# Kernel tuning notes

Measured on AMD Instinct MI355X. Metric: run time of the kernel, lower is better.

Reference implementation:

```python
import math
import jax, jax.numpy as jnp
import numpy as np

DIM = 1024
DIM_HEAD = 64
NUM_HEAD = 16
HIDDEN = DIM_HEAD * NUM_HEAD  # 1024
B, L = 4, 2048
EPS = 1e-12  # torch F.normalize eps


def rms_norm(x, g):
    # F.normalize(x, dim=-1) * g * sqrt(d): L2-normalize then rescale
    d = x.shape[-1]
    norm = jnp.maximum(jnp.linalg.norm(x, axis=-1, keepdims=True), EPS)
    return x / norm * g * math.sqrt(d)


def setup_inputs() -> dict:
    key = jax.random.key(0)
    ks = jax.random.split(key, 8)
    x = jax.random.normal(ks[0], (B, L, DIM), dtype=jnp.float32)
    # torch Linear init scale ~ 1/sqrt(fan_in)
    s1 = 1.0 / math.sqrt(DIM)
    s2 = 1.0 / math.sqrt(HIDDEN)
    Wqkv = jax.random.uniform(ks[1], (3 * HIDDEN, DIM), minval=-s1, maxval=s1, dtype=jnp.float32)
    bqkv = jax.random.uniform(ks[2], (3 * HIDDEN,), minval=-s1, maxval=s1, dtype=jnp.float32)
    Wout = jax.random.uniform(ks[3], (DIM, HIDDEN), minval=-s2, maxval=s2, dtype=jnp.float32)
    bout = jax.random.uniform(ks[4], (DIM,), minval=-s2, maxval=s2, dtype=jnp.float32)
    g_q = jnp.ones((HIDDEN,), dtype=jnp.float32)
    g_k = jnp.ones((HIDDEN,), dtype=jnp.float32)
    g_out = jnp.ones((DIM,), dtype=jnp.float32)
    return {"x": x, "Wqkv": Wqkv, "bqkv": bqkv, "Wout": Wout, "bout": bout,
            "g_q": g_q, "g_k": g_k, "g_out": g_out}


def reference(x, Wqkv, bqkv, Wout, bout, g_q, g_k, g_out):
    scale = DIM_HEAD ** -0.5
    qkv = x @ Wqkv.T + bqkv  # (b, l, 3*hidden)
    q, k, v = jnp.split(qkv, 3, axis=-1)
    # QK RMSNorm applied over flattened (num_head*d) channel dim
    q = rms_norm(q, g_q)
    k = rms_norm(k, g_k)
    split_heads = lambda t: t.reshape(B, L, NUM_HEAD, DIM_HEAD).transpose(0, 2, 1, 3)
    q, k, v = split_heads(q), split_heads(k), split_heads(v)  # (b, h, l, d)
    q = q * scale
    sim = jnp.einsum('bhld,bhnd->bhln', q, k)
    attn = jax.nn.softmax(sim, axis=-1)
    out = jnp.einsum('bhln,bhnd->bhld', attn, v)  # (b, h, l, d)
    out = out.transpose(0, 2, 1, 3).reshape(B, L, HIDDEN)  # b l (h d)
    out = out @ Wout.T + bout
    return rms_norm(out, g_out)
```

## Files before the change

### kernel.cpp

```cpp
#include <hip/hip_runtime.h>
#include <math.h>

#define DIM       1024
#define DIM_HEAD  64
#define NUM_HEAD  16
#define HIDDEN    1024
#define BATCH     4
#define SEQ       2048
#define ROWS      (BATCH * SEQ)
#define QKV_N     (3 * HIDDEN)
#define QK_N      2048

typedef __bf16 bf16_t;
typedef __bf16 bf16x8 __attribute__((ext_vector_type(8)));
typedef __bf16 bf16x4 __attribute__((ext_vector_type(4)));
typedef float  f32x4  __attribute__((ext_vector_type(4)));

#define F32_ONE_PATTERN 0x3F800000u
#define LOG2E 1.44269504088896f

#define GLOAD_LDS16(gp, lp)                                                  \
    __builtin_amdgcn_global_load_lds(                                        \
        (const __attribute__((address_space(1))) void*)(const void*)(gp),    \
        (__attribute__((address_space(3))) void*)(void*)(lp), 16, 0, 0)

__global__ __launch_bounds__(256) void decode_bf16(const void* __restrict__ in,
                                                   bf16_t* __restrict__ out,
                                                   const unsigned* __restrict__ sniff,
                                                   long n)
{
    const bool isf32 = (*sniff == F32_ONE_PATTERN);
    const long i = ((long)blockIdx.x * 256 + threadIdx.x) * 8;
    if (i >= n) return;
    if (isf32) {
        const float* p = (const float*)in + i;
        f32x4 a = *(const f32x4*)p;
        f32x4 b = *(const f32x4*)(p + 4);
        bf16x8 r;
        r[0] = (bf16_t)a[0]; r[1] = (bf16_t)a[1]; r[2] = (bf16_t)a[2]; r[3] = (bf16_t)a[3];
        r[4] = (bf16_t)b[0]; r[5] = (bf16_t)b[1]; r[6] = (bf16_t)b[2]; r[7] = (bf16_t)b[3];
        *(bf16x8*)&out[i] = r;
    } else {
        *(bf16x8*)&out[i] = *(const bf16x8*)((const bf16_t*)in + i);
    }
}

__global__ __launch_bounds__(256) void decode_params(
    const void* __restrict__ bqkv_raw, const void* __restrict__ bout_raw,
    const void* __restrict__ gq_raw,   const void* __restrict__ gk_raw,
    const void* __restrict__ gout_raw,
    float* __restrict__ o_bqkv, float* __restrict__ o_bout,
    float* __restrict__ o_gq,   float* __restrict__ o_gk,
    float* __restrict__ o_gout,
    const unsigned* __restrict__ sniff)
{
    const bool isf32 = (*sniff == F32_ONE_PATTERN);
    const int blk = blockIdx.x;
    const void* src; float* dst; int off;
    if (blk < 3)       { src = bqkv_raw; dst = o_bqkv; off = blk * 1024; }
    else if (blk == 3) { src = bout_raw; dst = o_bout; off = 0; }
    else if (blk == 4) { src = gq_raw;   dst = o_gq;   off = 0; }
    else if (blk == 5) { src = gk_raw;   dst = o_gk;   off = 0; }
    else               { src = gout_raw; dst = o_gout; off = 0; }
    const int i = off + threadIdx.x * 4;
    if (isf32) {
        *(f32x4*)&dst[i] = *((const f32x4*)src + (off >> 2) + threadIdx.x);
    } else {
        bf16x4 v = *((const bf16x4*)src + (off >> 2) + threadIdx.x);
        f32x4 a;
        a[0] = (float)v[0]; a[1] = (float)v[1]; a[2] = (float)v[2]; a[3] = (float)v[3];
        *(f32x4*)&dst[i] = a;
    }
}

__global__ __launch_bounds__(256) void gemm_qkv(
    const bf16_t* __restrict__ A,
    const bf16_t* __restrict__ Bt,
    const float*  __restrict__ bias,
    bf16_t* __restrict__ qk,
    bf16_t* __restrict__ vt)
{
    __shared__ __align__(16) bf16_t smem[8704];
    bf16_t* const As = smem;
    bf16_t* const Bs = smem + 4096;
    bf16_t* const Ts = smem;

    const int tid  = threadIdx.x;
    const int w    = tid >> 6;
    const int lane = tid & 63;
    const int wr   = w >> 1;
    const int wc   = w & 1;
    const int lr   = lane & 15;
    const int quad = lane >> 4;

    const int m0 = blockIdx.y * 128;
    const int n0 = blockIdx.x * 128;
    const int K  = DIM;

    const int e0 = tid * 8;
    const int r0 = e0 >> 5;
    const int c0 = e0 & 31;
    const int r1 = r0 + 64;

    f32x4 acc[4][4];
    #pragma unroll
    for (int i = 0; i < 4; i++)
        #pragma unroll
        for (int j = 0; j < 4; j++)
            acc[i][j] = (f32x4){0.f, 0.f, 0.f, 0.f};

    const bf16_t* pa0 = &A [(size_t)(m0 + r0) * K + c0];
    const bf16_t* pa1 = &A [(size_t)(m0 + r1) * K + c0];
    const bf16_t* pb0 = &Bt[(size_t)(n0 + r0) * K + c0];
    const bf16_t* pb1 = &Bt[(size_t)(n0 + r1) * K + c0];

    for (int k0 = 0; k0 < K; k0 += 32) {
        __syncthreads();
        GLOAD_LDS16(pa0 + k0, &As[e0]);
        GLOAD_LDS16(pa1 + k0, &As[e0 + 2048]);
        GLOAD_LDS16(pb0 + k0, &Bs[e0]);
        GLOAD_LDS16(pb1 + k0, &Bs[e0 + 2048]);
        __syncthreads();

        bf16x8 af[4], bfr[4];
        #pragma unroll
        for (int i = 0; i < 4; i++)
            af[i] = *(const bf16x8*)&As[(wr * 64 + i * 16 + lr) * 32 + quad * 8];
        #pragma unroll
        for (int j = 0; j < 4; j++)
            bfr[j] = *(const bf16x8*)&Bs[(wc * 64 + j * 16 + lr) * 32 + quad * 8];
        #pragma unroll
        for (int i = 0; i < 4; i++)
            #pragma unroll
            for (int j = 0; j < 4; j++)
                acc[i][j] = __builtin_amdgcn_mfma_f32_16x16x32_bf16(
                    af[i], bfr[j], acc[i][j], 0, 0, 0);
    }

    if (n0 < 2048) {
        #pragma unroll
        for (int i = 0; i < 4; i++) {
            const int row = m0 + wr * 64 + i * 16 + quad * 4;
            #pragma unroll
            for (int j = 0; j < 4; j++) {
                const int col = n0 + wc * 64 + j * 16 + lr;
                const float bv = bias[col];
                f32x4 v = acc[i][j];
                #pragma unroll
                for (int r = 0; r < 4; r++)
                    qk[(size_t)(row + r) * QK_N + col] = (bf16_t)(v[r] + bv);
            }
        }
    } else {
        const int b      = m0 >> 11;
        const int l_base = m0 & 2047;
        const int c_base = n0 - 2048;
        #pragma unroll
        for (int p = 0; p < 2; p++) {
            __syncthreads();
            if (wc == p) {
                #pragma unroll
                for (int j = 0; j < 4; j++) {
                    const int c = j * 16 + lr;
                    const float bv = bias[2048 + c_base + p * 64 + c];
                    #pragma unroll
                    for (int i = 0; i < 4; i++) {
                        const int l = wr * 64 + i * 16 + quad * 4;
                        f32x4 v = acc[i][j];
                        bf16x4 o;
                        o[0] = (bf16_t)(v[0] + bv);
                        o[1] = (bf16_t)(v[1] + bv);
                        o[2] = (bf16_t)(v[2] + bv);
                        o[3] = (bf16_t)(v[3] + bv);
                        *(bf16x4*)&Ts[c * 136 + l] = o;
                    }
                }
            }
            __syncthreads();
            const int c2 = tid >> 2, li = (tid & 3) * 32;
            const int cg = c_base + p * 64 + c2;
            const int h = cg >> 6, d = cg & 63;
            bf16_t* vrow = vt + ((size_t)((b << 4) | h) * 64 + d) * SEQ + l_base + li;
            #pragma unroll
            for (int e = 0; e < 4; e++)
                *(bf16x8*)&vrow[e * 8] = *(const bf16x8*)&Ts[c2 * 136 + li + e * 8];
        }
    }
}

__global__ __launch_bounds__(256) void gemm_out(
    const bf16_t* __restrict__ A,
    const bf16_t* __restrict__ Bt,
    const float*  __restrict__ bias,
    bf16_t* __restrict__ C)
{
    __shared__ __align__(16) bf16_t As[128 * 32];
    __shared__ __align__(16) bf16_t Bs[128 * 32];

    const int tid  = threadIdx.x;
    const int w    = tid >> 6;
    const int lane = tid & 63;
    const int wr   = w >> 1;
    const int wc   = w & 1;
    const int lr   = lane & 15;
    const int quad = lane >> 4;

    const int m0 = blockIdx.y * 128;
    const int n0 = blockIdx.x * 128;
    const int K  = HIDDEN;
    const int N  = DIM;

    const int e0 = tid * 8;
    const int r0 = e0 >> 5;
    const int c0 = e0 & 31;
    const int r1 = r0 + 64;

    f32x4 acc[4][4];
    #pragma unroll
    for (int i = 0; i < 4; i++)
        #pragma unroll
        for (int j = 0; j < 4; j++)
            acc[i][j] = (f32x4){0.f, 0.f, 0.f, 0.f};

    const bf16_t* pa0 = &A [(size_t)(m0 + r0) * K + c0];
    const bf16_t* pa1 = &A [(size_t)(m0 + r1) * K + c0];
    const bf16_t* pb0 = &Bt[(size_t)(n0 + r0) * K + c0];
    const bf16_t* pb1 = &Bt[(size_t)(n0 + r1) * K + c0];

    for (int k0 = 0; k0 < K; k0 += 32) {
        __syncthreads();
        GLOAD_LDS16(pa0 + k0, &As[e0]);
        GLOAD_LDS16(pa1 + k0, &As[e0 + 2048]);
        GLOAD_LDS16(pb0 + k0, &Bs[e0]);
        GLOAD_LDS16(pb1 + k0, &Bs[e0 + 2048]);
        __syncthreads();

        bf16x8 af[4], bfr[4];
        #pragma unroll
        for (int i = 0; i < 4; i++)
            af[i] = *(const bf16x8*)&As[(wr * 64 + i * 16 + lr) * 32 + quad * 8];
        #pragma unroll
        for (int j = 0; j < 4; j++)
            bfr[j] = *(const bf16x8*)&Bs[(wc * 64 + j * 16 + lr) * 32 + quad * 8];
        #pragma unroll
        for (int i = 0; i < 4; i++)
            #pragma unroll
            for (int j = 0; j < 4; j++)
                acc[i][j] = __builtin_amdgcn_mfma_f32_16x16x32_bf16(
                    af[i], bfr[j], acc[i][j], 0, 0, 0);
    }

    #pragma unroll
    for (int i = 0; i < 4; i++) {
        const int row = m0 + wr * 64 + i * 16 + quad * 4;
        #pragma unroll
        for (int j = 0; j < 4; j++) {
            const int col = n0 + wc * 64 + j * 16 + lr;
            const float bv = bias[col];
            f32x4 v = acc[i][j];
            #pragma unroll
            for (int r = 0; r < 4; r++)
                C[(size_t)(row + r) * N + col] = (bf16_t)(v[r] + bv);
        }
    }
}

__device__ __forceinline__ void norm_apply(bf16_t* __restrict__ row,
                                           const float* __restrict__ g,
                                           float mult, int tid, float* red)
{
    bf16x4 xv = *(const bf16x4*)&row[tid * 4];
    float f0 = (float)xv[0], f1 = (float)xv[1], f2 = (float)xv[2], f3 = (float)xv[3];
    float ss = f0 * f0 + f1 * f1 + f2 * f2 + f3 * f3;
    #pragma unroll
    for (int off = 32; off > 0; off >>= 1) ss += __shfl_xor(ss, off, 64);
    if ((tid & 63) == 0) red[tid >> 6] = ss;
    __syncthreads();
    const float tot  = red[0] + red[1] + red[2] + red[3];
    const float fac  = mult / fmaxf(sqrtf(tot), 1e-12f);
    f32x4 gv = *(const f32x4*)&g[tid * 4];
    bf16x4 o;
    o[0] = (bf16_t)(f0 * gv[0] * fac);
    o[1] = (bf16_t)(f1 * gv[1] * fac);
    o[2] = (bf16_t)(f2 * gv[2] * fac);
    o[3] = (bf16_t)(f3 * gv[3] * fac);
    *(bf16x4*)&row[tid * 4] = o;
    __syncthreads();
}

__global__ __launch_bounds__(256) void qk_rmsnorm(bf16_t* __restrict__ qk,
                                                  const float* __restrict__ gq,
                                                  const float* __restrict__ gk)
{
    __shared__ float red[4];
    const size_t base = (size_t)blockIdx.x * QK_N;
    norm_apply(qk + base, gq, 4.0f * LOG2E, threadIdx.x, red);
    norm_apply(qk + base + HIDDEN, gk, 32.0f, threadIdx.x, red);
}

__global__ __launch_bounds__(256) void final_rmsnorm(const bf16_t* __restrict__ in,
                                                     const float* __restrict__ g,
                                                     void* __restrict__ out,
                                                     const unsigned* __restrict__ sniff)
{
    __shared__ float red[4];
    const bool isf32 = (*sniff == F32_ONE_PATTERN);
    const int tid = threadIdx.x;
    const bf16_t* row = in + (size_t)blockIdx.x * HIDDEN;

    bf16x4 xv = *(const bf16x4*)&row[tid * 4];
    float f0 = (float)xv[0], f1 = (float)xv[1], f2 = (float)xv[2], f3 = (float)xv[3];
    float ss = f0 * f0 + f1 * f1 + f2 * f2 + f3 * f3;
    #pragma unroll
    for (int off = 32; off > 0; off >>= 1) ss += __shfl_xor(ss, off, 64);
    if ((tid & 63) == 0) red[tid >> 6] = ss;
    __syncthreads();
    const float tot = red[0] + red[1] + red[2] + red[3];
    const float fac = 32.0f / fmaxf(sqrtf(tot), 1e-12f);
    f32x4 gv = *(const f32x4*)&g[tid * 4];
    f32x4 o;
    o[0] = f0 * gv[0] * fac;
    o[1] = f1 * gv[1] * fac;
    o[2] = f2 * gv[2] * fac;
    o[3] = f3 * gv[3] * fac;
    if (isf32) {
        *(f32x4*)((float*)out + (size_t)blockIdx.x * HIDDEN + tid * 4) = o;
    } else {
        bf16x4 ob;
        ob[0] = (bf16_t)o[0]; ob[1] = (bf16_t)o[1];
        ob[2] = (bf16_t)o[2]; ob[3] = (bf16_t)o[3];
        *(bf16x4*)((bf16_t*)out + (size_t)blockIdx.x * HIDDEN + tid * 4) = ob;
    }
}

__global__ __launch_bounds__(256) void attn_mfma7(const bf16_t* __restrict__ qk,
                                                  const bf16_t* __restrict__ vt,
                                                  bf16_t* __restrict__ out)
{
    __shared__ __align__(16) union {
        bf16_t Ps[4][64 * 40];
        float  Obuf[2][64][68];
    } sh;
    __shared__ float lred[4][4][16];

    const int tid  = threadIdx.x;
    const int w    = tid >> 6;
    const int lane = tid & 63;
    const int l15  = lane & 15;
    const int quad = lane >> 4;

    const int j    = blockIdx.x;
    const int xcd  = j & 7;
    const int slot = j >> 3;
    const int bh   = ((slot >> 5) << 3) | xcd;
    const int q0   = (slot & 31) * 64;
    const int b = bh >> 4, h = bh & 15;

    bf16x8 qf[4][2];
    #pragma unroll
    for (int qt = 0; qt < 4; qt++) {
        const bf16_t* qrow = qk + (size_t)(b * SEQ + q0 + qt * 16 + l15) * QK_N + h * DIM_HEAD;
        qf[qt][0] = *(const bf16x8*)&qrow[quad * 8];
        qf[qt][1] = *(const bf16x8*)&qrow[32 + quad * 8];
    }

    f32x4 O[4][4];
    float lp[4] = {0.f, 0.f, 0.f, 0.f};
    #pragma unroll
    for (int qt = 0; qt < 4; qt++)
        #pragma unroll
        for (int dt = 0; dt < 4; dt++)
            O[qt][dt] = (f32x4){0.f, 0.f, 0.f, 0.f};

    const bf16_t* kptr = qk + (size_t)(b * SEQ + w * 32) * QK_N + HIDDEN + h * DIM_HEAD;
    const bf16_t* vptr = vt + (size_t)bh * 64 * SEQ + w * 32;
    const int koff0 = l15 * QK_N + quad * 8;
    const int koff1 = (16 + l15) * QK_N + quad * 8;
    const int voff  = l15 * SEQ + quad * 8;
    bf16_t* const psw = sh.Ps[w] + l15 * 40 + quad * 4;
    const bf16_t* const psr = sh.Ps[w] + l15 * 40 + quad * 8;

    for (int it = 0; it < SEQ / 128; it++) {
        bf16x8 kA[2][2], vB[4];
        kA[0][0] = *(const bf16x8*)(kptr + koff0);
        kA[0][1] = *(const bf16x8*)(kptr + koff0 + 32);
        kA[1][0] = *(const bf16x8*)(kptr + koff1);
        kA[1][1] = *(const bf16x8*)(kptr + koff1 + 32);
        #pragma unroll
        for (int dt = 0; dt < 4; dt++)
            vB[dt] = *(const bf16x8*)(vptr + voff + dt * 16 * SEQ);
        kptr += 128 * QK_N;
        vptr += 128;

        f32x4 s[2][4];
        #pragma unroll
        for (int kt = 0; kt < 2; kt++)
            #pragma unroll
            for (int qt = 0; qt < 4; qt++) {
                f32x4 z = (f32x4){0.f, 0.f, 0.f, 0.f};
                z = __builtin_amdgcn_mfma_f32_16x16x32_bf16(kA[kt][0], qf[qt][0], z, 0, 0, 0);
                s[kt][qt] = __builtin_amdgcn_mfma_f32_16x16x32_bf16(kA[kt][1], qf[qt][1], z, 0, 0, 0);
            }

        #pragma unroll
        for (int qt = 0; qt < 4; qt++)
            #pragma unroll
            for (int kt = 0; kt < 2; kt++) {
                bf16x4 pk;
                #pragma unroll
                for (int r = 0; r < 4; r++) {
                    const float p = __builtin_amdgcn_exp2f(s[kt][qt][r]);
                    lp[qt] += p;
                    pk[r] = (bf16_t)p;
                }
                *(bf16x4*)(psw + qt * 640 + kt * 16) = pk;
            }
        __builtin_amdgcn_s_waitcnt(0xC07F);

        #pragma unroll
        for (int qt = 0; qt < 4; qt++) {
            bf16x8 pf = *(const bf16x8*)(psr + qt * 640);
            #pragma unroll
            for (int dt = 0; dt < 4; dt++)
                O[qt][dt] = __builtin_amdgcn_mfma_f32_16x16x32_bf16(pf, vB[dt], O[qt][dt], 0, 0, 0);
        }
    }

    #pragma unroll
    for (int qt = 0; qt < 4; qt++) {
        lp[qt] += __shfl_xor(lp[qt], 16, 64);
        lp[qt] += __shfl_xor(lp[qt], 32, 64);
    }
    __syncthreads();
    if (w >= 2) {
        #pragma unroll
        for (int qt = 0; qt < 4; qt++)
            #pragma unroll
            for (int dt = 0; dt < 4; dt++)
                #pragma unroll
                for (int r = 0; r < 4; r++)
                    sh.Obuf[w - 2][qt * 16 + quad * 4 + r][dt * 16 + l15] = O[qt][dt][r];
    }
    if (quad == 0) {
        #pragma unroll
        for (int qt = 0; qt < 4; qt++) lred[w][qt][l15] = lp[qt];
    }
    __syncthreads();
    if (w < 2) {
        #pragma unroll
        for (int qt = 0; qt < 4; qt++)
            #pragma unroll
            for (int dt = 0; dt < 4; dt++)
                #pragma unroll
                for (int r = 0; r < 4; r++) {
                    float* p = &sh.Obuf[w][qt * 16 + quad * 4 + r][dt * 16 + l15];
                    *p += O[qt][dt][r];
                }
    }
    __syncthreads();
    #pragma unroll
    for (int i = 0; i < 2; i++) {
        const int u   = tid + i * 256;
        const int row = u >> 3;
        const int c8  = (u & 7) * 8;
        const float ls = lred[0][row >> 4][row & 15] + lred[1][row >> 4][row & 15]
                       + lred[2][row >> 4][row & 15] + lred[3][row >> 4][row & 15];
        const float inv = 1.0f / ls;
        f32x4 a0 = *(const f32x4*)&sh.Obuf[0][row][c8];
        f32x4 a1 = *(const f32x4*)&sh.Obuf[0][row][c8 + 4];
        f32x4 b0 = *(const f32x4*)&sh.Obuf[1][row][c8];
        f32x4 b1 = *(const f32x4*)&sh.Obuf[1][row][c8 + 4];
        bf16x8 o;
        o[0] = (bf16_t)((a0[0] + b0[0]) * inv);
        o[1] = (bf16_t)((a0[1] + b0[1]) * inv);
        o[2] = (bf16_t)((a0[2] + b0[2]) * inv);
        o[3] = (bf16_t)((a0[3] + b0[3]) * inv);
        o[4] = (bf16_t)((a1[0] + b1[0]) * inv);
        o[5] = (bf16_t)((a1[1] + b1[1]) * inv);
        o[6] = (bf16_t)((a1[2] + b1[2]) * inv);
        o[7] = (bf16_t)((a1[3] + b1[3]) * inv);
        *(bf16x8*)&out[(size_t)(b * SEQ + q0 + row) * HIDDEN + h * DIM_HEAD + c8] = o;
    }
}

extern "C" void kernel_launch(void* const* d_in, const int* in_sizes, int n_in,
                              void* d_out, int out_size, void* d_ws, size_t ws_size,
                              hipStream_t stream)
{
    (void)in_sizes; (void)n_in; (void)out_size; (void)ws_size;
    const void* x_raw    = d_in[0];
    const void* Wqkv_raw = d_in[1];
    const void* bqkv_raw = d_in[2];
    const void* Wout_raw = d_in[3];
    const void* bout_raw = d_in[4];
    const void* gq_raw   = d_in[5];
    const void* gk_raw   = d_in[6];
    const void* gout_raw = d_in[7];
    const unsigned* sniff = (const unsigned*)d_in[5];

    char* ws = (char*)d_ws;
    bf16_t* xb      = (bf16_t*)(ws + 0);
    bf16_t* Wqkvb   = (bf16_t*)(ws + (16l << 20));
    bf16_t* Woutb   = (bf16_t*)(ws + (22l << 20));
    float*  bqkv_f  = (float*) (ws + (24l << 20));
    float*  bout_f  = (float*) (ws + (24l << 20) + 16384);
    float*  gq_f    = (float*) (ws + (24l << 20) + 2 * 16384);
    float*  gk_f    = (float*) (ws + (24l << 20) + 3 * 16384);
    float*  gout_f  = (float*) (ws + (24l << 20) + 4 * 16384);
    bf16_t* qk      = (bf16_t*)(ws + (25l << 20));
    bf16_t* vtb     = (bf16_t*)(ws + (57l << 20));
    bf16_t* attn_o  = xb;
    bf16_t* out_b   = qk;

    decode_bf16<<<(ROWS * DIM) / 2048, 256, 0, stream>>>(x_raw, xb, sniff, (long)ROWS * DIM);
    decode_bf16<<<(QKV_N * DIM) / 2048, 256, 0, stream>>>(Wqkv_raw, Wqkvb, sniff, (long)QKV_N * DIM);
    decode_bf16<<<(DIM * HIDDEN) / 2048, 256, 0, stream>>>(Wout_raw, Woutb, sniff, (long)DIM * HIDDEN);
    decode_params<<<7, 256, 0, stream>>>(bqkv_raw, bout_raw, gq_raw, gk_raw, gout_raw,
                                         bqkv_f, bout_f, gq_f, gk_f, gout_f, sniff);

    gemm_qkv<<<dim3(QKV_N / 128, ROWS / 128), 256, 0, stream>>>(
        xb, Wqkvb, bqkv_f, qk, vtb);
    qk_rmsnorm<<<ROWS, 256, 0, stream>>>(qk, gq_f, gk_f);
    attn_mfma7<<<(SEQ / 64) * BATCH * NUM_HEAD, 256, 0, stream>>>(qk, vtb, attn_o);
    gemm_out<<<dim3(DIM / 128, ROWS / 128), 256, 0, stream>>>(
        attn_o, Woutb, bout_f, out_b);
    final_rmsnorm<<<ROWS, 256, 0, stream>>>(out_b, gout_f, d_out, sniff);
}
```

Measured before the change: 364.7 us.

## Double-buffer K tiles through LDS with async global-to-LDS loads in attention

The attention kernel now stages each wave's 32-row K tile into a per-wave double-buffered LDS region using global_load_lds, prefetching the next iteration's tile while the current one is consumed. The LDS layout uses a rotation swizzle to avoid bank conflicts on the fragment reads. This targets the exposed latency of loading K fragments directly from global memory each iteration. It adds 32 KB of LDS per block, which may reduce occupancy, and the hand-coded waitcnt immediate must correctly order the async loads.

```diff
diff --git a/kernel.cpp b/kernel.cpp
--- a/kernel.cpp
+++ b/kernel.cpp
@@ -333,10 +333,11 @@
     }
 }
 
-__global__ __launch_bounds__(256) void attn_mfma7(const bf16_t* __restrict__ qk,
+__global__ __launch_bounds__(256) void attn_mfma9(const bf16_t* __restrict__ qk,
                                                   const bf16_t* __restrict__ vt,
                                                   bf16_t* __restrict__ out)
 {
+    __shared__ __align__(16) bf16_t Ks[4][2][2048];
     __shared__ __align__(16) union {
         bf16_t Ps[4][64 * 40];
         float  Obuf[2][64][68];
@@ -372,25 +373,48 @@
         for (int dt = 0; dt < 4; dt++)
             O[qt][dt] = (f32x4){0.f, 0.f, 0.f, 0.f};
 
-    const bf16_t* kptr = qk + (size_t)(b * SEQ + w * 32) * QK_N + HIDDEN + h * DIM_HEAD;
+    const int r8  = lane >> 3;
+    const int c8l = lane & 7;
+    const int srccol = ((c8l * 8 + (r8 & 3) * 16) & 63);
+    const bf16_t* kstage = qk + (size_t)(b * SEQ + w * 32) * QK_N + HIDDEN + h * DIM_HEAD
+                         + r8 * QK_N + srccol;
+    bf16_t* const ksb = &Ks[w][0][0];
+
+    const int swz0 = ((quad * 8 + 64 - (l15 & 3) * 16) & 63);
+    const int swz1 = ((32 + quad * 8 + 64 - (l15 & 3) * 16) & 63);
+    const int krow = l15 * 64;
+
+    #pragma unroll
+    for (int t = 0; t < 4; t++)
+        GLOAD_LDS16(kstage + t * 8 * QK_N, ksb + t * 512);
+    kstage += 128 * QK_N;
+
     const bf16_t* vptr = vt + (size_t)bh * 64 * SEQ + w * 32;
-    const int koff0 = l15 * QK_N + quad * 8;
-    const int koff1 = (16 + l15) * QK_N + quad * 8;
-    const int voff  = l15 * SEQ + quad * 8;
+    const int voff = l15 * SEQ + quad * 8;
     bf16_t* const psw = sh.Ps[w] + l15 * 40 + quad * 4;
     const bf16_t* const psr = sh.Ps[w] + l15 * 40 + quad * 8;
 
     for (int it = 0; it < SEQ / 128; it++) {
-        bf16x8 kA[2][2], vB[4];
-        kA[0][0] = *(const bf16x8*)(kptr + koff0);
-        kA[0][1] = *(const bf16x8*)(kptr + koff0 + 32);
-        kA[1][0] = *(const bf16x8*)(kptr + koff1);
-        kA[1][1] = *(const bf16x8*)(kptr + koff1 + 32);
+        const int cur = (it & 1) * 2048;
+        const int nxt = 2048 - cur;
+        __builtin_amdgcn_s_waitcnt(0x0F70);
+
+        bf16x8 vB[4];
         #pragma unroll
         for (int dt = 0; dt < 4; dt++)
             vB[dt] = *(const bf16x8*)(vptr + voff + dt * 16 * SEQ);
-        kptr += 128 * QK_N;
         vptr += 128;
+
+        bf16x8 kA[2][2];
+        kA[0][0] = *(const bf16x8*)&ksb[cur + krow + swz0];
+        kA[0][1] = *(const bf16x8*)&ksb[cur + krow + swz1];
+        kA[1][0] = *(const bf16x8*)&ksb[cur + 1024 + krow + swz0];
+        kA[1][1] = *(const bf16x8*)&ksb[cur + 1024 + krow + swz1];
+
+        #pragma unroll
+        for (int t = 0; t < 4; t++)
+            GLOAD_LDS16(kstage + t * 8 * QK_N, ksb + nxt + t * 512);
+        kstage += 128 * QK_N;
 
         f32x4 s[2][4];
         #pragma unroll
@@ -521,7 +545,7 @@
     gemm_qkv<<<dim3(QKV_N / 128, ROWS / 128), 256, 0, stream>>>(
         xb, Wqkvb, bqkv_f, qk, vtb);
     qk_rmsnorm<<<ROWS, 256, 0, stream>>>(qk, gq_f, gk_f);
-    attn_mfma7<<<(SEQ / 64) * BATCH * NUM_HEAD, 256, 0, stream>>>(qk, vtb, attn_o);
+    attn_mfma9<<<(SEQ / 64) * BATCH * NUM_HEAD, 256, 0, stream>>>(qk, vtb, attn_o);
     gemm_out<<<dim3(DIM / 128, ROWS / 128), 256, 0, stream>>>(
         attn_o, Woutb, bout_f, out_b);
     final_rmsnorm<<<ROWS, 256, 0, stream>>>(out_b, gout_f, d_out, sniff);
```

Measured after the change: 330.8 us. 1.1x faster.
